# Kernel tuning notes

Hardware: AMD Instinct MI355X
Metric: run time of the kernel (lower is better)

## Reference

```python
import jax, jax.numpy as jnp
import numpy as np

NUM_USER = 1_000_000
NUM_ITEM = 100_000
HIDDEN = 64
NUM_PAIRS = 2_000_000


def setup_inputs() -> dict:
    key = jax.random.key(0)
    k1, k2, k3, k4 = jax.random.split(key, 4)
    user_emb = jax.random.normal(k1, (NUM_USER, HIDDEN), dtype=jnp.float32)
    item_emb = jax.random.normal(k2, (NUM_ITEM, HIDDEN), dtype=jnp.float32)
    user_ids = jax.random.randint(k3, (NUM_PAIRS,), 0, NUM_USER, dtype=jnp.int32)
    item_ids = jax.random.randint(k4, (NUM_PAIRS,), 0, NUM_ITEM, dtype=jnp.int32)
    return {"user_emb": user_emb, "item_emb": item_emb,
            "user_ids": user_ids, "item_ids": item_ids}


def reference(user_emb, item_emb, user_ids, item_ids):
    # PMF rating prediction: relu(<U[u], V[i]>) for each observed (u, i) pair.
    u = user_emb[user_ids]          # [P, D] gather
    v = item_emb[item_ids]          # [P, D] gather
    ratings = jnp.einsum('pd,pd->p', u, v)  # per-pair dot product
    return jax.nn.relu(ratings)
```

## Files before the change

kernel.cpp:

```cpp
#include <hip/hip_runtime.h>


constexpr int HIDDEN = 64;
constexpr int K = 4;

__global__ __launch_bounds__(256) void pmf_dot_kernel(
    const float* __restrict__ user_emb,
    const float* __restrict__ item_emb,
    const int*   __restrict__ user_ids,
    const int*   __restrict__ item_ids,
    float*       __restrict__ out,
    int n_pairs)
{
    const int group  = (blockIdx.x * blockDim.x + threadIdx.x) >> 4;
    const int lane16 = threadIdx.x & 15;
    const int p0     = group * K;

    if (p0 + K <= n_pairs) {
        const int4 u4 = *reinterpret_cast<const int4*>(user_ids + p0);
        const int4 i4 = *reinterpret_cast<const int4*>(item_ids + p0);

        const float4* up0 = reinterpret_cast<const float4*>(user_emb + (size_t)u4.x * HIDDEN) + lane16;
        const float4* up1 = reinterpret_cast<const float4*>(user_emb + (size_t)u4.y * HIDDEN) + lane16;
        const float4* up2 = reinterpret_cast<const float4*>(user_emb + (size_t)u4.z * HIDDEN) + lane16;
        const float4* up3 = reinterpret_cast<const float4*>(user_emb + (size_t)u4.w * HIDDEN) + lane16;
        const float4* vp0 = reinterpret_cast<const float4*>(item_emb + (size_t)i4.x * HIDDEN) + lane16;
        const float4* vp1 = reinterpret_cast<const float4*>(item_emb + (size_t)i4.y * HIDDEN) + lane16;
        const float4* vp2 = reinterpret_cast<const float4*>(item_emb + (size_t)i4.z * HIDDEN) + lane16;
        const float4* vp3 = reinterpret_cast<const float4*>(item_emb + (size_t)i4.w * HIDDEN) + lane16;

        const float4 a0 = *up0, a1 = *up1, a2 = *up2, a3 = *up3;
        const float4 b0 = *vp0, b1 = *vp1, b2 = *vp2, b3 = *vp3;

        float d0 = a0.x * b0.x + a0.y * b0.y + a0.z * b0.z + a0.w * b0.w;
        float d1 = a1.x * b1.x + a1.y * b1.y + a1.z * b1.z + a1.w * b1.w;
        float d2 = a2.x * b2.x + a2.y * b2.y + a2.z * b2.z + a2.w * b2.w;
        float d3 = a3.x * b3.x + a3.y * b3.y + a3.z * b3.z + a3.w * b3.w;

        #pragma unroll
        for (int s = 1; s < 16; s <<= 1) {
            d0 += __shfl_xor(d0, s, 16);
            d1 += __shfl_xor(d1, s, 16);
            d2 += __shfl_xor(d2, s, 16);
            d3 += __shfl_xor(d3, s, 16);
        }

        if (lane16 == 0) {
            float4 r;
            r.x = d0 > 0.0f ? d0 : 0.0f;
            r.y = d1 > 0.0f ? d1 : 0.0f;
            r.z = d2 > 0.0f ? d2 : 0.0f;
            r.w = d3 > 0.0f ? d3 : 0.0f;
            *reinterpret_cast<float4*>(out + p0) = r;
        }
    } else if (p0 < n_pairs) {
        for (int p = p0; p < n_pairs; ++p) {
            const int uid = user_ids[p];
            const int iid = item_ids[p];
            const float4 a = *(reinterpret_cast<const float4*>(user_emb + (size_t)uid * HIDDEN) + lane16);
            const float4 b = *(reinterpret_cast<const float4*>(item_emb + (size_t)iid * HIDDEN) + lane16);
            float d = a.x * b.x + a.y * b.y + a.z * b.z + a.w * b.w;
            #pragma unroll
            for (int s = 1; s < 16; s <<= 1) d += __shfl_xor(d, s, 16);
            if (lane16 == 0) out[p] = d > 0.0f ? d : 0.0f;
        }
    }
}

extern "C" void kernel_launch(void* const* d_in, const int* in_sizes, int n_in,
                              void* d_out, int out_size, void* d_ws, size_t ws_size,
                              hipStream_t stream) {
    const float* user_emb = (const float*)d_in[0];
    const float* item_emb = (const float*)d_in[1];
    const int*   user_ids = (const int*)d_in[2];
    const int*   item_ids = (const int*)d_in[3];
    float* out = (float*)d_out;

    const int n_pairs = in_sizes[2];
    const int threads = 256;
    const int pairs_per_block = (threads / 16) * K;
    const int blocks = (n_pairs + pairs_per_block - 1) / pairs_per_block;

    pmf_dot_kernel<<<blocks, threads, 0, stream>>>(
        user_emb, item_emb, user_ids, item_ids, out, n_pairs);
}
```

Baseline: 420.9 us.

## Bin pairs by user-id range before gathering to improve embedding locality

Adds a counting-sort pipeline (per-chunk histogram, scan, scatter) that groups pairs into 512 buckets by user-id range, then runs a binned dot-product kernel so blocks gather user rows from a narrow region of the user table. The aim is better L2 and MALL locality for the 256 MB user table. In exchange it adds three extra launches, a 32 MB triple write and read, a single-block serial scan, and scattered output writes. Load balance across fixed-size bucket blocks depends on a uniform id distribution.

```diff
diff --git a/kernel.cpp b/kernel.cpp
--- a/kernel.cpp
+++ b/kernel.cpp
@@ -3,6 +3,10 @@
 
 constexpr int HIDDEN = 64;
 constexpr int K = 4;
+constexpr int MAX_BUCKETS = 512;
+constexpr int BASE_CHUNK = 4096;
+
+using uint = unsigned int;
 
 __global__ __launch_bounds__(256) void pmf_dot_kernel(
     const float* __restrict__ user_emb,
@@ -67,6 +71,129 @@
     }
 }
 
+__global__ __launch_bounds__(256) void chunk_hist_kernel(
+    const int* __restrict__ uids, uint* __restrict__ chunkhist,
+    int n, int chunk, int shift)
+{
+    __shared__ uint h[MAX_BUCKETS];
+    for (int i = threadIdx.x; i < MAX_BUCKETS; i += 256) h[i] = 0u;
+    __syncthreads();
+    const int start = blockIdx.x * chunk;
+    const int end   = min(start + chunk, n);
+    for (int i = start + threadIdx.x; i < end; i += 256) {
+        const uint b = min(((uint)uids[i]) >> shift, (uint)(MAX_BUCKETS - 1));
+        atomicAdd(&h[b], 1u);
+    }
+    __syncthreads();
+    for (int i = threadIdx.x; i < MAX_BUCKETS; i += 256)
+        chunkhist[(size_t)blockIdx.x * MAX_BUCKETS + i] = h[i];
+}
+
+__global__ __launch_bounds__(MAX_BUCKETS) void scan_kernel(
+    const uint* __restrict__ chunkhist, uint* __restrict__ chunkbase,
+    uint* __restrict__ offsets, int nchunks)
+{
+    const int b = threadIdx.x;
+    uint acc = 0u;
+    for (int c = 0; c < nchunks; ++c) {
+        chunkbase[(size_t)c * MAX_BUCKETS + b] = acc;
+        acc += chunkhist[(size_t)c * MAX_BUCKETS + b];
+    }
+    __shared__ uint tmp[MAX_BUCKETS];
+    tmp[b] = acc;
+    __syncthreads();
+    for (int d = 1; d < MAX_BUCKETS; d <<= 1) {
+        uint v = (b >= d) ? tmp[b - d] : 0u;
+        __syncthreads();
+        tmp[b] += v;
+        __syncthreads();
+    }
+    const uint start = b ? tmp[b - 1] : 0u;
+    offsets[b] = start;
+    if (b == MAX_BUCKETS - 1) offsets[MAX_BUCKETS] = tmp[b];
+    for (int c = 0; c < nchunks; ++c)
+        chunkbase[(size_t)c * MAX_BUCKETS + b] += start;
+}
+
+__global__ __launch_bounds__(256) void scatter_kernel(
+    const int* __restrict__ uids, const int* __restrict__ iids,
+    const uint* __restrict__ chunkbase, int4* __restrict__ triples,
+    int n, int chunk, int shift)
+{
+    __shared__ uint base[MAX_BUCKETS];
+    __shared__ uint lcnt[MAX_BUCKETS];
+    for (int i = threadIdx.x; i < MAX_BUCKETS; i += 256) {
+        base[i] = chunkbase[(size_t)blockIdx.x * MAX_BUCKETS + i];
+        lcnt[i] = 0u;
+    }
+    __syncthreads();
+    const int start = blockIdx.x * chunk;
+    const int end   = min(start + chunk, n);
+    for (int i = start + threadIdx.x; i < end; i += 256) {
+        const int u = uids[i];
+        const int v = iids[i];
+        const uint b = min(((uint)u) >> shift, (uint)(MAX_BUCKETS - 1));
+        const uint slot = base[b] + atomicAdd(&lcnt[b], 1u);
+        if (slot < (uint)n)
+            triples[slot] = make_int4(u, v, i, 0);
+    }
+}
+
+__global__ __launch_bounds__(256) void pmf_binned_kernel(
+    const float* __restrict__ user_emb,
+    const float* __restrict__ item_emb,
+    const uint*  __restrict__ offsets,
+    const int4*  __restrict__ triples,
+    float*       __restrict__ out)
+{
+    const int bucket = blockIdx.x >> 2;
+    const uint s = offsets[bucket];
+    const uint e = offsets[bucket + 1];
+    const int lane16 = threadIdx.x & 15;
+    const int g = ((blockIdx.x & 3) << 4) | (threadIdx.x >> 4);
+
+    for (uint q = s + (uint)g * 4u; q < e; q += 256u) {
+        uint idx = q + (uint)(lane16 & 3);
+        if (idx >= e) idx = e - 1;
+        const int4 t = triples[idx];
+
+        const int u0 = __shfl(t.x, 0, 16), i0 = __shfl(t.y, 0, 16);
+        const int u1 = __shfl(t.x, 1, 16), i1 = __shfl(t.y, 1, 16);
+        const int u2 = __shfl(t.x, 2, 16), i2 = __shfl(t.y, 2, 16);
+        const int u3 = __shfl(t.x, 3, 16), i3 = __shfl(t.y, 3, 16);
+
+        const float4* up0 = reinterpret_cast<const float4*>(user_emb + (size_t)u0 * HIDDEN) + lane16;
+        const float4* up1 = reinterpret_cast<const float4*>(user_emb + (size_t)u1 * HIDDEN) + lane16;
+        const float4* up2 = reinterpret_cast<const float4*>(user_emb + (size_t)u2 * HIDDEN) + lane16;
+        const float4* up3 = reinterpret_cast<const float4*>(user_emb + (size_t)u3 * HIDDEN) + lane16;
+        const float4* vp0 = reinterpret_cast<const float4*>(item_emb + (size_t)i0 * HIDDEN) + lane16;
+        const float4* vp1 = reinterpret_cast<const float4*>(item_emb + (size_t)i1 * HIDDEN) + lane16;
+        const float4* vp2 = reinterpret_cast<const float4*>(item_emb + (size_t)i2 * HIDDEN) + lane16;
+        const float4* vp3 = reinterpret_cast<const float4*>(item_emb + (size_t)i3 * HIDDEN) + lane16;
+
+        const float4 a0 = *up0, a1 = *up1, a2 = *up2, a3 = *up3;
+        const float4 b0 = *vp0, b1 = *vp1, b2 = *vp2, b3 = *vp3;
+
+        float d0 = a0.x * b0.x + a0.y * b0.y + a0.z * b0.z + a0.w * b0.w;
+        float d1 = a1.x * b1.x + a1.y * b1.y + a1.z * b1.z + a1.w * b1.w;
+        float d2 = a2.x * b2.x + a2.y * b2.y + a2.z * b2.z + a2.w * b2.w;
+        float d3 = a3.x * b3.x + a3.y * b3.y + a3.z * b3.z + a3.w * b3.w;
+
+        #pragma unroll
+        for (int sft = 1; sft < 16; sft <<= 1) {
+            d0 += __shfl_xor(d0, sft, 16);
+            d1 += __shfl_xor(d1, sft, 16);
+            d2 += __shfl_xor(d2, sft, 16);
+            d3 += __shfl_xor(d3, sft, 16);
+        }
+
+        if (lane16 < 4 && (q + (uint)lane16) < e) {
+            const float d = lane16 == 0 ? d0 : lane16 == 1 ? d1 : lane16 == 2 ? d2 : d3;
+            out[t.z] = d > 0.0f ? d : 0.0f;
+        }
+    }
+}
+
 extern "C" void kernel_launch(void* const* d_in, const int* in_sizes, int n_in,
                               void* d_out, int out_size, void* d_ws, size_t ws_size,
                               hipStream_t stream) {
@@ -77,10 +204,38 @@
     float* out = (float*)d_out;
 
     const int n_pairs = in_sizes[2];
-    const int threads = 256;
-    const int pairs_per_block = (threads / 16) * K;
-    const int blocks = (n_pairs + pairs_per_block - 1) / pairs_per_block;
-
-    pmf_dot_kernel<<<blocks, threads, 0, stream>>>(
-        user_emb, item_emb, user_ids, item_ids, out, n_pairs);
-}
+
+    long long n_users = (long long)in_sizes[0] / HIDDEN;
+    int shift = 11;
+    while (n_users > 0 && (((n_users - 1) >> shift) >= MAX_BUCKETS)) ++shift;
+
+    int chunk = BASE_CHUNK;
+    while ((n_pairs + chunk - 1) / chunk > MAX_BUCKETS) chunk <<= 1;
+    const int nchunks = (n_pairs + chunk - 1) / chunk;
+
+    const size_t META = 4096 + 2ull * MAX_BUCKETS * MAX_BUCKETS * sizeof(uint);
+    const size_t ws_need = META + (size_t)n_pairs * sizeof(int4);
+
+    if (d_ws == nullptr || ws_size < ws_need || n_pairs < BASE_CHUNK) {
+        const int threads = 256;
+        const int pairs_per_block = (threads / 16) * K;
+        const int blocks = (n_pairs + pairs_per_block - 1) / pairs_per_block;
+        pmf_dot_kernel<<<blocks, threads, 0, stream>>>(
+            user_emb, item_emb, user_ids, item_ids, out, n_pairs);
+        return;
+    }
+
+    uint* offsets   = (uint*)d_ws;
+    uint* chunkhist = (uint*)((char*)d_ws + 4096);
+    uint* chunkbase = chunkhist + (size_t)MAX_BUCKETS * MAX_BUCKETS;
+    int4* triples   = (int4*)((char*)d_ws + META);
+
+    chunk_hist_kernel<<<nchunks, 256, 0, stream>>>(
+        user_ids, chunkhist, n_pairs, chunk, shift);
+    scan_kernel<<<1, MAX_BUCKETS, 0, stream>>>(
+        chunkhist, chunkbase, offsets, nchunks);
+    scatter_kernel<<<nchunks, 256, 0, stream>>>(
+        user_ids, item_ids, chunkbase, triples, n_pairs, chunk, shift);
+    pmf_binned_kernel<<<MAX_BUCKETS * 4, 256, 0, stream>>>(
+        user_emb, item_emb, offsets, triples, out);
+}
```

Measured after the change: 714.8 us. 1.7x slower.
